# Kernel tuning notes

Hardware: AMD Instinct MI355X
Metric: run time of the kernel (lower is better)

## Reference

```python
import jax, jax.numpy as jnp
import numpy as np

L, N, E, H, D, F = 2048, 2, 1024, 16, 64, 4096  # seq, batch, embed, heads, head_dim, ffn
EPS = 1e-5


def _ln(x, w, b):
    m = jnp.mean(x, axis=-1, keepdims=True)
    v = jnp.mean(jnp.square(x - m), axis=-1, keepdims=True)
    return (x - m) * jax.lax.rsqrt(v + EPS) * w + b


def setup_inputs() -> dict:
    key = jax.random.key(0)
    ks = jax.random.split(key, 16)
    s = 0.02
    f32 = jnp.float32
    return {
        "x": jax.random.normal(ks[0], (L, N, E), f32),
        "ln1_w": jnp.ones((E,), f32),
        "ln1_b": jnp.zeros((E,), f32),
        "wq": jax.random.normal(ks[1], (H * D, E), f32) * s,
        "bq": jnp.zeros((H * D,), f32),
        "wk": jax.random.normal(ks[2], (H * D, E), f32) * s,
        "bk": jnp.zeros((H * D,), f32),
        "wv": jax.random.normal(ks[3], (H * D, E), f32) * s,
        "bv": jnp.zeros((H * D,), f32),
        "wout": jax.random.normal(ks[4], (E, H * D), f32) * s,
        "bout": jnp.zeros((E,), f32),
        "ln2_w": jnp.ones((E,), f32),
        "ln2_b": jnp.zeros((E,), f32),
        "fc1_w": jax.random.normal(ks[5], (F, E), f32) * s,
        "fc1_b": jnp.zeros((F,), f32),
        "fc2_w": jax.random.normal(ks[6], (E, F), f32) * s,
        "fc2_b": jnp.zeros((E,), f32),
    }


def reference(x, ln1_w, ln1_b, wq, bq, wk, bk, wv, bv, wout, bout,
              ln2_w, ln2_b, fc1_w, fc1_b, fc2_w, fc2_b):
    scale = D ** (-0.5)
    residual = x
    h = _ln(x, ln1_w, ln1_b)                      # (L,N,E)
    q = (h @ wq.T + bq).reshape(L, N, H, D) * scale
    k = (h @ wk.T + bk).reshape(L, N, H, D)
    v = (h @ wv.T + bv).reshape(L, N, H, D)
    attn = jnp.einsum('qnhd,knhd->nhqk', q, k)    # (N,H,L,L) full score matrix
    causal = jnp.tril(jnp.ones((L, L), bool))
    attn = jnp.where(causal[None, None], attn, jnp.float32(-10000.0))
    p = jax.nn.softmax(attn, axis=-1)
    o = jnp.einsum('nhqk,knhd->qnhd', p, v).reshape(L, N, H * D)
    o = o @ wout.T + bout
    x = o + residual
    residual = x
    h = _ln(x, ln2_w, ln2_b)
    h = jax.nn.gelu(h @ fc1_w.T + fc1_b, approximate=False)
    h = h @ fc2_w.T + fc2_b
    return h + residual
```

## Files before the change

### kernel.cpp

```cpp
#include <hip/hip_runtime.h>
#include <hip/hip_bf16.h>
#include <math.h>

using bf16 = __hip_bfloat16;
typedef __bf16 bf16x8 __attribute__((ext_vector_type(8)));
typedef short  short4v __attribute__((ext_vector_type(4)));
typedef float  f32x4  __attribute__((ext_vector_type(4)));

static constexpr int Lq = 2048, Nb = 2, E = 1024, Hh = 16, Dd = 64, Ff = 4096;
static constexpr int MT = Lq * Nb;
static constexpr int QKLD = 2 * E;
static constexpr int LDL = 2 * QKLD;

__device__ __forceinline__ void async_lds16(const void* g, void* l) {
  __builtin_amdgcn_global_load_lds(
      (const __attribute__((address_space(1))) void*)g,
      (__attribute__((address_space(3))) void*)l, 16, 0, 0);
}
__device__ __forceinline__ bf16x8 ld8(const bf16* p) { return *(const bf16x8*)p; }
__device__ __forceinline__ short bfbits(float x) {
  bf16 t = __float2bfloat16(x);
  return *(short*)&t;
}
__device__ __forceinline__ float gelu_fast(float v) {
  const float y = fminf(2.302208f * (v + 0.044715f * v * v * v), 80.f);
  const float t = exp2f(y);
  return v * t / (t + 1.0f);
}

__global__ __launch_bounds__(256) void cvt_all_kernel(
    const float* __restrict__ wq, const float* __restrict__ wk,
    const float* __restrict__ wv, const float* __restrict__ wout,
    const float* __restrict__ fc1w, const float* __restrict__ fc2w,
    bf16* __restrict__ wqkvb, bf16* __restrict__ woutb,
    bf16* __restrict__ f1wb, bf16* __restrict__ f2wb) {
  const int i = blockIdx.x * 256 + threadIdx.x;
  const float* src;
  bf16* dst;
  size_t off;
  if (i < 786432) {
    const int r = i >> 18;
    off = (size_t)(i & 262143);
    src = (r == 0) ? wq : (r == 1) ? wk : wv;
    dst = wqkvb + (size_t)r * (E * E);
  } else if (i < 1048576) {
    off = (size_t)(i - 786432); src = wout; dst = woutb;
  } else if (i < 2097152) {
    off = (size_t)(i - 1048576); src = fc1w; dst = f1wb;
  } else {
    off = (size_t)(i - 2097152); src = fc2w; dst = f2wb;
  }
  float4 v = ((const float4*)src)[off];
  bf16 o4[4] = {__float2bfloat16(v.x), __float2bfloat16(v.y),
                __float2bfloat16(v.z), __float2bfloat16(v.w)};
  *(uint2*)(dst + 4 * off) = *(uint2*)o4;
}

template <int EPI>
__global__ __launch_bounds__(256) void gemm_bt(
    const bf16* __restrict__ A, const bf16* __restrict__ W,
    const float* __restrict__ b1, const float* __restrict__ b2,
    const float* __restrict__ b3, int Klen, int Kstride, int Nld,
    float qscale, int scut, bf16* __restrict__ outb,
    bf16* __restrict__ outv) {
  __shared__ __align__(16) bf16 As[128 * 64];
  __shared__ __align__(16) bf16 Bs[128 * 64];
  const int tid = threadIdx.x;
  const int w = tid >> 6, lane = tid & 63;
  const int quad = lane >> 4, l16 = lane & 15;
  const int wm = (w >> 1) * 64, wn = (w & 1) * 64;
  const int m0 = blockIdx.y * 128, n0 = blockIdx.x * 128;
  const int koff = blockIdx.z * Klen;

  f32x4 acc[4][4];
#pragma unroll
  for (int i = 0; i < 4; i++)
#pragma unroll
    for (int j = 0; j < 4; j++)
#pragma unroll
      for (int r = 0; r < 4; r++) acc[i][j][r] = 0.f;

  const int rowoff = w * 8 + (lane >> 3);
  const int colsw = (((lane & 7) ^ (lane >> 3)) << 3);

  const int nk = Klen >> 6;
  for (int kt = 0; kt < nk; ++kt) {
    const int k0 = koff + (kt << 6);
#pragma unroll
    for (int r = 0; r < 4; r++) {
      async_lds16(A + (size_t)(m0 + r * 32 + rowoff) * Kstride + k0 + colsw,
                  As + (size_t)(r * 256 + w * 64) * 8);
      async_lds16(W + (size_t)(n0 + r * 32 + rowoff) * Kstride + k0 + colsw,
                  Bs + (size_t)(r * 256 + w * 64) * 8);
    }
    __syncthreads();
#pragma unroll
    for (int ksub = 0; ksub < 2; ksub++) {
      const int gx = ksub * 4 + quad;
      bf16x8 a[4], b[4];
#pragma unroll
      for (int i = 0; i < 4; i++) {
        const int ra = wm + i * 16 + l16;
        const int rb = wn + i * 16 + l16;
        a[i] = ld8(&As[(size_t)(ra * 8 + (gx ^ (l16 & 7))) * 8]);
        b[i] = ld8(&Bs[(size_t)(rb * 8 + (gx ^ (l16 & 7))) * 8]);
      }
#pragma unroll
      for (int i = 0; i < 4; i++)
#pragma unroll
        for (int j = 0; j < 4; j++)
          acc[i][j] = __builtin_amdgcn_mfma_f32_16x16x32_bf16(a[i], b[j], acc[i][j], 0, 0, 0);
    }
    __syncthreads();
  }

  const size_t zoff = (EPI == 3) ? (size_t)blockIdx.z * ((size_t)MT * E) : 0;
#pragma unroll
  for (int i = 0; i < 4; i++) {
    const int mrow = m0 + wm + i * 16 + quad * 4;
#pragma unroll
    for (int j = 0; j < 4; j++) {
      const int ncol = n0 + wn + j * 16 + l16;
      float bv = 0.f;
      if constexpr (EPI != 3) {
        if (b3 != nullptr) {
          bv = (ncol < 1024) ? b1[ncol]
               : (ncol < 2048) ? b2[ncol - 1024] : b3[ncol - 2048];
        } else {
          bv = b1[ncol];
        }
      }
      const float sc = (ncol < scut) ? qscale : 1.0f;
#pragma unroll
      for (int r = 0; r < 4; r++) {
        float v = (acc[i][j][r] + bv) * sc;
        if constexpr (EPI == 2) {
          outb[(size_t)(mrow + r) * Nld + ncol] = __float2bfloat16(gelu_fast(v));
        } else if constexpr (EPI == 3) {
          outb[zoff + (size_t)(mrow + r) * Nld + ncol] = __float2bfloat16(v);
        } else {
          if (ncol < 2048) {
            outb[(size_t)(mrow + r) * 2048 + ncol] = __float2bfloat16(v);
          } else {
            const int h = (ncol - 2048) >> 6, d = ncol & 63;
            const int tok = mrow + r, n = tok & 1, l = tok >> 1;
            outv[(size_t)((n * 16 + h) * 64 + d) * Lq + l] = __float2bfloat16(v);
          }
        }
      }
    }
  }
}

__global__ __launch_bounds__(256) void reduce2_kernel(
    const bf16* __restrict__ P, const float* __restrict__ bias,
    const float* __restrict__ res, float* __restrict__ out) {
  const int i = blockIdx.x * 256 + threadIdx.x;
  const size_t e0 = (size_t)i * 4;
  const int col = (int)(e0 & (E - 1));
  uint2 u0 = *(const uint2*)(P + e0);
  uint2 u1 = *(const uint2*)(P + (size_t)MT * E + e0);
  const bf16* p0 = (const bf16*)&u0;
  const bf16* p1 = (const bf16*)&u1;
  float4 b = *(const float4*)(bias + col);
  float4 r = *(const float4*)(res + e0);
  float4 o;
  o.x = (float)p0[0] + (float)p1[0] + b.x + r.x;
  o.y = (float)p0[1] + (float)p1[1] + b.y + r.y;
  o.z = (float)p0[2] + (float)p1[2] + b.z + r.z;
  o.w = (float)p0[3] + (float)p1[3] + b.w + r.w;
  *(float4*)(out + e0) = o;
}

__global__ __launch_bounds__(256) void redln_kernel(
    const bf16* __restrict__ P, const float* __restrict__ bias,
    const float* __restrict__ res, const float* __restrict__ wgt,
    const float* __restrict__ bia, float* __restrict__ x1,
    bf16* __restrict__ h2) {
  const int t = blockIdx.x, tid = threadIdx.x;
  const size_t base = (size_t)t * E;
  const int e0 = tid * 4;
  uint2 u0 = *(const uint2*)(P + base + e0);
  uint2 u1 = *(const uint2*)(P + (size_t)MT * E + base + e0);
  const bf16* p0 = (const bf16*)&u0;
  const bf16* p1 = (const bf16*)&u1;
  float4 b = *(const float4*)(bias + e0);
  float4 r = *(const float4*)(res + base + e0);
  float v4[4];
  v4[0] = (float)p0[0] + (float)p1[0] + b.x + r.x;
  v4[1] = (float)p0[1] + (float)p1[1] + b.y + r.y;
  v4[2] = (float)p0[2] + (float)p1[2] + b.z + r.z;
  v4[3] = (float)p0[3] + (float)p1[3] + b.w + r.w;
  *(float4*)(x1 + base + e0) = *(float4*)v4;

  float s = 0.f, ss = 0.f;
#pragma unroll
  for (int i = 0; i < 4; i++) { s += v4[i]; ss += v4[i] * v4[i]; }
  for (int off = 32; off > 0; off >>= 1) {
    s += __shfl_down(s, off, 64);
    ss += __shfl_down(ss, off, 64);
  }
  __shared__ float rs[4], rss[4], mv[2];
  const int w = tid >> 6;
  if ((tid & 63) == 0) { rs[w] = s; rss[w] = ss; }
  __syncthreads();
  if (tid == 0) {
    float S = rs[0] + rs[1] + rs[2] + rs[3];
    float SS = rss[0] + rss[1] + rss[2] + rss[3];
    float mean = S * (1.f / E);
    float var = SS * (1.f / E) - mean * mean;
    mv[0] = mean; mv[1] = rsqrtf(var + 1e-5f);
  }
  __syncthreads();
  const float mean = mv[0], rstd = mv[1];
  float4 wg = *(const float4*)(wgt + e0);
  float4 bb = *(const float4*)(bia + e0);
  bf16 o4[4];
  o4[0] = __float2bfloat16((v4[0] - mean) * rstd * wg.x + bb.x);
  o4[1] = __float2bfloat16((v4[1] - mean) * rstd * wg.y + bb.y);
  o4[2] = __float2bfloat16((v4[2] - mean) * rstd * wg.z + bb.z);
  o4[3] = __float2bfloat16((v4[3] - mean) * rstd * wg.w + bb.w);
  *(uint2*)(h2 + base + e0) = *(uint2*)o4;
}

__global__ __launch_bounds__(256) void ln_kernel(
    const float* __restrict__ x, const float* __restrict__ wgt,
    const float* __restrict__ bia, bf16* __restrict__ out) {
  const int t = blockIdx.x, tid = threadIdx.x;
  const size_t base = (size_t)t * E;
  float v4[4], s = 0.f, ss = 0.f;
#pragma unroll
  for (int i = 0; i < 4; i++) {
    float v = x[base + i * 256 + tid];
    v4[i] = v; s += v; ss += v * v;
  }
  for (int off = 32; off > 0; off >>= 1) {
    s += __shfl_down(s, off, 64);
    ss += __shfl_down(ss, off, 64);
  }
  __shared__ float rs[4], rss[4], mv[2];
  const int w = tid >> 6;
  if ((tid & 63) == 0) { rs[w] = s; rss[w] = ss; }
  __syncthreads();
  if (tid == 0) {
    float S = rs[0] + rs[1] + rs[2] + rs[3];
    float SS = rss[0] + rss[1] + rss[2] + rss[3];
    float mean = S * (1.f / E);
    float var = SS * (1.f / E) - mean * mean;
    mv[0] = mean; mv[1] = rsqrtf(var + 1e-5f);
  }
  __syncthreads();
  const float mean = mv[0], rstd = mv[1];
#pragma unroll
  for (int i = 0; i < 4; i++) {
    const int e = i * 256 + tid;
    float r = (v4[i] - mean) * rstd * wgt[e] + bia[e];
    out[base + e] = __float2bfloat16(r);
  }
}

__global__ __launch_bounds__(256) void attn_kernel(
    const bf16* __restrict__ QK, const bf16* __restrict__ VT,
    bf16* __restrict__ O) {
  __shared__ __align__(16) bf16 KB[512 * 8];
  __shared__ __align__(16) bf16 VB[512 * 8];
  const int tid = threadIdx.x;
  const int w = tid >> 6, lane = tid & 63, quad = lane >> 4, l16 = lane & 15;
  const int pid = blockIdx.x;
  const int hh = blockIdx.y;
  const int n = hh >> 4, h = hh & 15;

  const bf16* Qp = QK + n * QKLD + h * Dd;
  const bf16* Kp = Qp + E;
  const bf16* Vp = VT + (size_t)hh * 64 * Lq;

  bf16* ldsK0 = KB + (size_t)(w * 64) * 8;
  bf16* ldsK1 = KB + (size_t)(256 + w * 64) * 8;
  bf16* ldsV0 = VB + (size_t)(w * 64) * 8;
  bf16* ldsV1 = VB + (size_t)(256 + w * 64) * 8;
  const int w8 = w * 8;

  for (int half = 0; half < 2; ++half) {
    const int qt = (half == 0) ? (31 - pid) : pid;
    const int ql = qt * 64 + w * 16 + l16;
    const bf16x8 aq0 = ld8(Qp + (size_t)ql * LDL + quad * 8);
    const bf16x8 aq1 = ld8(Qp + (size_t)ql * LDL + 32 + quad * 8);

    f32x4 o_acc[4];
#pragma unroll
    for (int d = 0; d < 4; d++)
#pragma unroll
      for (int r = 0; r < 4; r++) o_acc[d][r] = 0.f;
    float m_run = -3e30f, l_run = 0.f;

    for (int kt = 0; kt <= qt; ++kt) {
      const size_t kb = (size_t)kt * 64;

      async_lds16(Kp + (size_t)(kb + lane) * LDL + w8, ldsK0);
      async_lds16(Kp + (size_t)(kb + lane) * LDL + 32 + w8, ldsK1);
      async_lds16(Vp + (size_t)lane * Lq + kb + w8, ldsV0);
      async_lds16(Vp + (size_t)lane * Lq + kb + 32 + w8, ldsV1);
      __syncthreads();

      f32x4 s[4];
#pragma unroll
      for (int ks = 0; ks < 4; ks++) {
        const bf16x8 kc0 = ld8(&KB[(size_t)((quad)*64 + ks * 16 + l16) * 8]);
        const bf16x8 kc1 = ld8(&KB[(size_t)((4 + quad) * 64 + ks * 16 + l16) * 8]);
#pragma unroll
        for (int r = 0; r < 4; r++) s[ks][r] = 0.f;
        s[ks] = __builtin_amdgcn_mfma_f32_16x16x32_bf16(kc0, aq0, s[ks], 0, 0, 0);
        s[ks] = __builtin_amdgcn_mfma_f32_16x16x32_bf16(kc1, aq1, s[ks], 0, 0, 0);
      }

      if (kt == qt) {
#pragma unroll
        for (int ks = 0; ks < 4; ks++) {
#pragma unroll
          for (int r = 0; r < 4; r++) {
            const int kg = kt * 64 + ks * 16 + quad * 4 + r;
            if (kg > ql) s[ks][r] = -14427.0f;
          }
        }
      }

      float tmax = s[0][0];
#pragma unroll
      for (int ks = 0; ks < 4; ks++)
#pragma unroll
        for (int r = 0; r < 4; r++) tmax = fmaxf(tmax, s[ks][r]);
      tmax = fmaxf(tmax, __shfl_xor(tmax, 16, 64));
      tmax = fmaxf(tmax, __shfl_xor(tmax, 32, 64));
      const float mnew = fmaxf(m_run, tmax);
      const float alpha = exp2f(m_run - mnew);
      m_run = mnew;
      float rsum = 0.f;
      short4v pf[4];
#pragma unroll
      for (int ks = 0; ks < 4; ks++) {
#pragma unroll
        for (int r = 0; r < 4; r++) {
          const float pv = exp2f(s[ks][r] - mnew);
          rsum += pv;
          pf[ks][r] = bfbits(pv);
        }
      }
      rsum += __shfl_xor(rsum, 16, 64);
      rsum += __shfl_xor(rsum, 32, 64);
      l_run = l_run * alpha + rsum;
#pragma unroll
      for (int d = 0; d < 4; d++)
#pragma unroll
        for (int r = 0; r < 4; r++) o_acc[d][r] *= alpha;

#pragma unroll
      for (int d = 0; d < 4; d++) {
#pragma unroll
        for (int ks = 0; ks < 4; ks++) {
          const int g = ks * 2 + (quad >> 1);
          const short4v av =
              *(const short4v*)&VB[(size_t)(g * 64 + d * 16 + l16) * 8 + (quad & 1) * 4];
          o_acc[d] = __builtin_amdgcn_mfma_f32_16x16x16bf16_1k(av, pf[ks], o_acc[d], 0, 0, 0);
        }
      }
      __syncthreads();
    }

    const float inv_l = 1.f / fmaxf(l_run, 1e-30f);
    const size_t obase = (size_t)ql * (Nb * E) + (size_t)n * E + h * Dd;
#pragma unroll
    for (int d = 0; d < 4; d++)
#pragma unroll
      for (int r = 0; r < 4; r++)
        O[obase + d * 16 + quad * 4 + r] = __float2bfloat16(o_acc[d][r] * inv_l);
  }
}

extern "C" void kernel_launch(void* const* d_in, const int* in_sizes, int n_in,
                              void* d_out, int out_size, void* d_ws, size_t ws_size,
                              hipStream_t stream) {
  const float* x    = (const float*)d_in[0];
  const float* ln1w = (const float*)d_in[1];
  const float* ln1b = (const float*)d_in[2];
  const float* wq   = (const float*)d_in[3];
  const float* bq   = (const float*)d_in[4];
  const float* wk   = (const float*)d_in[5];
  const float* bk   = (const float*)d_in[6];
  const float* wv   = (const float*)d_in[7];
  const float* bv   = (const float*)d_in[8];
  const float* wout = (const float*)d_in[9];
  const float* bout = (const float*)d_in[10];
  const float* ln2w = (const float*)d_in[11];
  const float* ln2b = (const float*)d_in[12];
  const float* fc1w = (const float*)d_in[13];
  const float* fc1b = (const float*)d_in[14];
  const float* fc2w = (const float*)d_in[15];
  const float* fc2b = (const float*)d_in[16];

  char* ws = (char*)d_ws;
  bf16* wqkvb = (bf16*)(ws);
  bf16* woutb = (bf16*)(ws + ((size_t)6 << 20));
  bf16* f1wb  = (bf16*)(ws + ((size_t)8 << 20));
  bf16* f2wb  = (bf16*)(ws + ((size_t)16 << 20));
  bf16* h1    = (bf16*)(ws + ((size_t)24 << 20));
  bf16* qk    = (bf16*)(ws + ((size_t)32 << 20));
  bf16* vtg   = (bf16*)(ws + ((size_t)48 << 20));
  bf16* o     = (bf16*)(ws + ((size_t)56 << 20));
  float* x1   = (float*)(ws + ((size_t)64 << 20));
  bf16* Pout  = (bf16*)(ws + ((size_t)32 << 20));
  bf16* P01   = (bf16*)(ws);
  bf16* f1    = (bf16*)(ws + ((size_t)32 << 20));
  bf16* h2    = h1;
  float* outp = (float*)d_out;

  cvt_all_kernel<<<12288, 256, 0, stream>>>(wq, wk, wv, wout, fc1w, fc2w,
                                            wqkvb, woutb, f1wb, f2wb);

  ln_kernel<<<MT, 256, 0, stream>>>(x, ln1w, ln1b, h1);

  dim3 gQKV(3 * E / 128, MT / 128);
  dim3 gE2(E / 128, MT / 128, 2);
  dim3 gF(Ff / 128, MT / 128);

  gemm_bt<4><<<gQKV, 256, 0, stream>>>(h1, wqkvb, bq, bk, bv, E, E, 2048,
                                       0.125f * 1.44269504f, 1024, qk, vtg);

  attn_kernel<<<dim3(16, Nb * Hh), 256, 0, stream>>>(qk, vtg, o);

  gemm_bt<3><<<gE2, 256, 0, stream>>>(o, woutb, nullptr, nullptr, nullptr,
                                      E / 2, E, E, 1.f, 0, Pout, nullptr);
  redln_kernel<<<MT, 256, 0, stream>>>(Pout, bout, x, ln2w, ln2b, x1, h2);

  gemm_bt<2><<<gF, 256, 0, stream>>>(h2, f1wb, fc1b, nullptr, nullptr, E, E, Ff,
                                     1.f, 0, f1, nullptr);

  gemm_bt<3><<<gE2, 256, 0, stream>>>(f1, f2wb, nullptr, nullptr, nullptr,
                                      Ff / 2, Ff, E, 1.f, 0, P01, nullptr);
  reduce2_kernel<<<MT * E / 1024, 256, 0, stream>>>(P01, fc2b, x1, outp);
}
```

Measured before the change: 380.5 us.

## Add BK=32 GEMM path for FC1 and remap attention grid across XCDs

Templates the GEMM on K-tile depth and adds a BK=32 variant with a simpler unswizzled LDS layout, used only for the FC1 GEMM. This halves LDS use per block, which may allow more resident blocks, at the cost of twice as many barriers per K and possible LDS bank conflicts from the unswizzled reads. It also flattens the attention launch to a 1D grid and remaps block IDs so the 16 query-tile blocks of a head land on the same XCD, aiming for better L2 reuse of that head's K and V.

```diff
diff --git a/kernel.cpp b/kernel.cpp
--- a/kernel.cpp
+++ b/kernel.cpp
@@ -56,15 +56,15 @@
   *(uint2*)(dst + 4 * off) = *(uint2*)o4;
 }
 
-template <int EPI>
+template <int EPI, int BK>
 __global__ __launch_bounds__(256) void gemm_bt(
     const bf16* __restrict__ A, const bf16* __restrict__ W,
     const float* __restrict__ b1, const float* __restrict__ b2,
     const float* __restrict__ b3, int Klen, int Kstride, int Nld,
     float qscale, int scut, bf16* __restrict__ outb,
     bf16* __restrict__ outv) {
-  __shared__ __align__(16) bf16 As[128 * 64];
-  __shared__ __align__(16) bf16 Bs[128 * 64];
+  __shared__ __align__(16) bf16 As[128 * BK];
+  __shared__ __align__(16) bf16 Bs[128 * BK];
   const int tid = threadIdx.x;
   const int w = tid >> 6, lane = tid & 63;
   const int quad = lane >> 4, l16 = lane & 15;
@@ -80,38 +80,72 @@
 #pragma unroll
       for (int r = 0; r < 4; r++) acc[i][j][r] = 0.f;
 
-  const int rowoff = w * 8 + (lane >> 3);
-  const int colsw = (((lane & 7) ^ (lane >> 3)) << 3);
-
-  const int nk = Klen >> 6;
-  for (int kt = 0; kt < nk; ++kt) {
-    const int k0 = koff + (kt << 6);
-#pragma unroll
-    for (int r = 0; r < 4; r++) {
-      async_lds16(A + (size_t)(m0 + r * 32 + rowoff) * Kstride + k0 + colsw,
-                  As + (size_t)(r * 256 + w * 64) * 8);
-      async_lds16(W + (size_t)(n0 + r * 32 + rowoff) * Kstride + k0 + colsw,
-                  Bs + (size_t)(r * 256 + w * 64) * 8);
-    }
-    __syncthreads();
-#pragma unroll
-    for (int ksub = 0; ksub < 2; ksub++) {
-      const int gx = ksub * 4 + quad;
+  if constexpr (BK == 32) {
+    const int c0 = w * 64 + lane;
+    const int c1 = c0 + 256;
+    const size_t arow0 = (size_t)(m0 + (c0 >> 2)), arow1 = (size_t)(m0 + (c1 >> 2));
+    const size_t brow0 = (size_t)(n0 + (c0 >> 2)), brow1 = (size_t)(n0 + (c1 >> 2));
+    const int col0 = (c0 & 3) * 8, col1 = (c1 & 3) * 8;
+    bf16* ldsA0 = &As[(w * 64) * 8];
+    bf16* ldsA1 = &As[(256 + w * 64) * 8];
+    bf16* ldsB0 = &Bs[(w * 64) * 8];
+    bf16* ldsB1 = &Bs[(256 + w * 64) * 8];
+
+    const int nk = Klen >> 5;
+    for (int kt = 0; kt < nk; ++kt) {
+      const int k0 = koff + kt * 32;
+      async_lds16(A + arow0 * Kstride + k0 + col0, ldsA0);
+      async_lds16(A + arow1 * Kstride + k0 + col1, ldsA1);
+      async_lds16(W + brow0 * Kstride + k0 + col0, ldsB0);
+      async_lds16(W + brow1 * Kstride + k0 + col1, ldsB1);
+      __syncthreads();
       bf16x8 a[4], b[4];
 #pragma unroll
       for (int i = 0; i < 4; i++) {
-        const int ra = wm + i * 16 + l16;
-        const int rb = wn + i * 16 + l16;
-        a[i] = ld8(&As[(size_t)(ra * 8 + (gx ^ (l16 & 7))) * 8]);
-        b[i] = ld8(&Bs[(size_t)(rb * 8 + (gx ^ (l16 & 7))) * 8]);
+        a[i] = ld8(&As[(wm + i * 16 + l16) * 32 + quad * 8]);
+        b[i] = ld8(&Bs[(wn + i * 16 + l16) * 32 + quad * 8]);
       }
 #pragma unroll
       for (int i = 0; i < 4; i++)
 #pragma unroll
         for (int j = 0; j < 4; j++)
           acc[i][j] = __builtin_amdgcn_mfma_f32_16x16x32_bf16(a[i], b[j], acc[i][j], 0, 0, 0);
+      __syncthreads();
     }
-    __syncthreads();
+  } else {
+    const int rowoff = w * 8 + (lane >> 3);
+    const int colsw = (((lane & 7) ^ (lane >> 3)) << 3);
+
+    const int nk = Klen >> 6;
+    for (int kt = 0; kt < nk; ++kt) {
+      const int k0 = koff + (kt << 6);
+#pragma unroll
+      for (int r = 0; r < 4; r++) {
+        async_lds16(A + (size_t)(m0 + r * 32 + rowoff) * Kstride + k0 + colsw,
+                    As + (size_t)(r * 256 + w * 64) * 8);
+        async_lds16(W + (size_t)(n0 + r * 32 + rowoff) * Kstride + k0 + colsw,
+                    Bs + (size_t)(r * 256 + w * 64) * 8);
+      }
+      __syncthreads();
+#pragma unroll
+      for (int ksub = 0; ksub < 2; ksub++) {
+        const int gx = ksub * 4 + quad;
+        bf16x8 a[4], b[4];
+#pragma unroll
+        for (int i = 0; i < 4; i++) {
+          const int ra = wm + i * 16 + l16;
+          const int rb = wn + i * 16 + l16;
+          a[i] = ld8(&As[(size_t)(ra * 8 + (gx ^ (l16 & 7))) * 8]);
+          b[i] = ld8(&Bs[(size_t)(rb * 8 + (gx ^ (l16 & 7))) * 8]);
+        }
+#pragma unroll
+        for (int i = 0; i < 4; i++)
+#pragma unroll
+          for (int j = 0; j < 4; j++)
+            acc[i][j] = __builtin_amdgcn_mfma_f32_16x16x32_bf16(a[i], b[j], acc[i][j], 0, 0, 0);
+      }
+      __syncthreads();
+    }
   }
 
   const size_t zoff = (EPI == 3) ? (size_t)blockIdx.z * ((size_t)MT * E) : 0;
@@ -266,8 +300,11 @@
   __shared__ __align__(16) bf16 VB[512 * 8];
   const int tid = threadIdx.x;
   const int w = tid >> 6, lane = tid & 63, quad = lane >> 4, l16 = lane & 15;
-  const int pid = blockIdx.x;
-  const int hh = blockIdx.y;
+  const int bid = blockIdx.x;
+  const int xcd = bid & 7;
+  const int inner = bid >> 3;
+  const int pid = inner & 15;
+  const int hh = ((inner >> 4) << 3) | xcd;
   const int n = hh >> 4, h = hh & 15;
 
   const bf16* Qp = QK + n * QKLD + h * Dd;
@@ -422,19 +459,19 @@
   dim3 gE2(E / 128, MT / 128, 2);
   dim3 gF(Ff / 128, MT / 128);
 
-  gemm_bt<4><<<gQKV, 256, 0, stream>>>(h1, wqkvb, bq, bk, bv, E, E, 2048,
-                                       0.125f * 1.44269504f, 1024, qk, vtg);
-
-  attn_kernel<<<dim3(16, Nb * Hh), 256, 0, stream>>>(qk, vtg, o);
-
-  gemm_bt<3><<<gE2, 256, 0, stream>>>(o, woutb, nullptr, nullptr, nullptr,
-                                      E / 2, E, E, 1.f, 0, Pout, nullptr);
+  gemm_bt<4, 64><<<gQKV, 256, 0, stream>>>(h1, wqkvb, bq, bk, bv, E, E, 2048,
+                                           0.125f * 1.44269504f, 1024, qk, vtg);
+
+  attn_kernel<<<512, 256, 0, stream>>>(qk, vtg, o);
+
+  gemm_bt<3, 64><<<gE2, 256, 0, stream>>>(o, woutb, nullptr, nullptr, nullptr,
+                                          E / 2, E, E, 1.f, 0, Pout, nullptr);
   redln_kernel<<<MT, 256, 0, stream>>>(Pout, bout, x, ln2w, ln2b, x1, h2);
 
-  gemm_bt<2><<<gF, 256, 0, stream>>>(h2, f1wb, fc1b, nullptr, nullptr, E, E, Ff,
-                                     1.f, 0, f1, nullptr);
-
-  gemm_bt<3><<<gE2, 256, 0, stream>>>(f1, f2wb, nullptr, nullptr, nullptr,
-                                      Ff / 2, Ff, E, 1.f, 0, P01, nullptr);
+  gemm_bt<2, 32><<<gF, 256, 0, stream>>>(h2, f1wb, fc1b, nullptr, nullptr,
+                                         E, E, Ff, 1.f, 0, f1, nullptr);
+
+  gemm_bt<3, 64><<<gE2, 256, 0, stream>>>(f1, f2wb, nullptr, nullptr, nullptr,
+                                          Ff / 2, Ff, E, 1.f, 0, P01, nullptr);
   reduce2_kernel<<<MT * E / 1024, 256, 0, stream>>>(P01, fc2b, x1, outp);
 }
```

Result: no change. 380.9 us (+0.1%).
